# Kernel tuning notes

Measured on AMD Instinct MI355X. Metric: run time of the kernel, lower is better.

Reference implementation:

```python
import jax, jax.numpy as jnp
import numpy as np

B, N, A, T = 65536, 128, 32, 64


def setup_inputs() -> dict:
    key = jax.random.key(0)
    k1, k2, k3, k4 = jax.random.split(key, 4)
    traj = jax.random.normal(k1, (B, N, 3), dtype=jnp.float32)
    ref_x = jax.random.normal(k2, (A, 3), dtype=jnp.float32)
    ref_x = ref_x - jnp.mean(ref_x, axis=0, keepdims=True)  # centered ref, as in __init__
    align_idx = jnp.sort(jax.random.randint(k3, (A,), 0, N)).astype(jnp.int64)
    train_idx = jnp.sort(jax.random.randint(k4, (T,), 0, N)).astype(jnp.int64)
    return {"traj": traj, "ref_x": ref_x, "align_idx": align_idx, "train_idx": train_idx}


def reference(traj, ref_x, align_idx, train_idx):
    # --- Kabsch alignment ---
    sel = traj[:, align_idx, :]                      # [B, A, 3]
    x_c = jnp.mean(sel, axis=1, keepdims=True)       # [B, 1, 3]
    x0 = sel - x_c                                   # centered selection
    # prod = x0^T @ ref_x : [B, 3, 3]
    prod = jnp.einsum('bai,aj->bij', x0, ref_x)
    u, s, vh = jnp.linalg.svd(prod)                  # batched 3x3 SVD
    # proper-rotation sign fix (det of u @ vh), detached in the original
    sign = jax.lax.stop_gradient(jnp.sign(jnp.linalg.det(jnp.matmul(u, vh))))  # [B]
    d = jnp.stack([jnp.ones_like(sign), jnp.ones_like(sign), sign], axis=-1)   # [B, 3]
    rotate = jnp.matmul(u * d[:, None, :], vh)       # u @ diag(1,1,sign) @ vh, [B,3,3]
    aligned = jnp.matmul(traj - x_c, rotate)         # [B, N, 3]
    # --- select train atoms and flatten ---
    out = aligned[:, train_idx, :].reshape(traj.shape[0], -1)  # [B, T*3]
    return out
```

## Files before the change

kernel.cpp:

```cpp
#include <hip/hip_runtime.h>
#include <math.h>

#define N_ATOMS  128
#define A_ALIGN  32
#define T_TRAIN  64
#define ROWF     (N_ATOMS*3)
#define R4       (ROWF/4)
#define BPBLK    64
#define PPW      8

template<int p, int q, int r>
__device__ __forceinline__ void jrot(float Am[3][3], float Vm[3][3])
{
    float apq = Am[p][q];
    float app = Am[p][p];
    float aqq = Am[q][q];
    float tau = (aqq - app) / (2.0f * apq);
    float tt  = 1.0f / (fabsf(tau) + sqrtf(1.0f + tau * tau));
    float t   = copysignf(tt, tau);
    t = (fabsf(apq) > 1e-20f) ? t : 0.0f;
    float c = 1.0f / sqrtf(1.0f + t * t);
    float s = t * c;
    float arp = Am[r][p], arq = Am[r][q];
    float nrp = c * arp - s * arq;
    float nrq = s * arp + c * arq;
    Am[r][p] = nrp; Am[p][r] = nrp;
    Am[r][q] = nrq; Am[q][r] = nrq;
    Am[p][p] = app - t * apq;
    Am[q][q] = aqq + t * apq;
    Am[p][q] = 0.0f; Am[q][p] = 0.0f;
#pragma unroll
    for (int k = 0; k < 3; ++k) {
        float vp = Vm[k][p], vq = Vm[k][q];
        Vm[k][p] = c * vp - s * vq;
        Vm[k][q] = s * vp + c * vq;
    }
}

__device__ __forceinline__ float redu32(float v)
{
#pragma unroll
    for (int m = 16; m >= 1; m >>= 1)
        v += __shfl_xor(v, m, 32);
    return v;
}

__global__ __launch_bounds__(256)
void kabsch_onepass_kernel(const float* __restrict__ traj,
                           const float* __restrict__ ref_x,
                           const int*   __restrict__ align_idx,
                           const int*   __restrict__ train_idx,
                           float*       __restrict__ out,
                           int B)
{
    __shared__ float slice[4][2 * ROWF];
    __shared__ float Pbuf[BPBLK][12];

    const int tid = threadIdx.x;
    const int w  = tid >> 6;
    const int l  = tid & 63;
    const int h  = l >> 5;
    const int tp = l & 31;

    const long long bbase = (long long)blockIdx.x * BPBLK;

    const int   ia = align_idx[tp];
    const float rx = ref_x[tp*3+0], ry = ref_x[tp*3+1], rz = ref_x[tp*3+2];
    const int   ti0 = train_idx[tp];
    const int   ti1 = train_idx[tp + 32];

    const float4* __restrict__ g4 = (const float4*)traj;
    const long long maxf4 = (long long)B * R4;
    float4* s4 = (float4*)slice[w];
    const float* __restrict__ rb = &slice[w][h * ROWF];

#pragma unroll 1
    for (int it = 0; it < PPW; ++it) {
        int pl = w * PPW + it;
        long long b = bbase + (long long)pl * 2;
        if (b >= B) break;
        long long fb = b * R4;
        long long i0 = fb + l;        if (i0 >= maxf4) i0 = maxf4 - 1;
        long long i1 = fb + 64 + l;   if (i1 >= maxf4) i1 = maxf4 - 1;
        long long i2 = fb + 128 + l;  if (i2 >= maxf4) i2 = maxf4 - 1;
        float4 v0 = g4[i0];
        float4 v1 = g4[i1];
        float4 v2 = g4[i2];
        s4[l]       = v0;
        s4[64 + l]  = v1;
        s4[128 + l] = v2;

        float px = rb[ia*3+0], py = rb[ia*3+1], pz = rb[ia*3+2];

        float S00 = redu32(px*rx), S01 = redu32(px*ry), S02 = redu32(px*rz);
        float S10 = redu32(py*rx), S11 = redu32(py*ry), S12 = redu32(py*rz);
        float S20 = redu32(pz*rx), S21 = redu32(pz*ry), S22 = redu32(pz*rz);
        float xs0 = redu32(px), xs1 = redu32(py), xs2 = redu32(pz);
        float rs0 = redu32(rx), rs1 = redu32(ry), rs2 = redu32(rz);

        if (tp == 0 && (b + h) < B) {
            const float inv_a = 1.0f / (float)A_ALIGN;
            float c0 = xs0*inv_a, c1 = xs1*inv_a, c2 = xs2*inv_a;
            float4* o4 = (float4*)Pbuf[pl*2 + h];
            o4[0] = make_float4(S00 - c0*rs0, S01 - c0*rs1, S02 - c0*rs2,
                                S10 - c1*rs0);
            o4[1] = make_float4(S11 - c1*rs1, S12 - c1*rs2, S20 - c2*rs0,
                                S21 - c2*rs1);
            o4[2] = make_float4(S22 - c2*rs2, c0, c1, c2);
        }
    }
    __syncthreads();

    const int cw = blockIdx.x & 3;
    if ((tid >> 6) == cw && (bbase + (tid & 63)) < B) {
        const int r = tid & 63;
        float4* w4 = (float4*)Pbuf[r];
        float4 q0 = w4[0], q1 = w4[1], q2 = w4[2];
        float P00=q0.x, P01=q0.y, P02=q0.z, P10=q0.w;
        float P11=q1.x, P12=q1.y, P20=q1.z, P21=q1.w;
        float P22=q2.x, c0=q2.y, c1=q2.z, c2=q2.w;

        float Am[3][3], Vm[3][3];
        Am[0][0] = P00*P00 + P10*P10 + P20*P20;
        Am[0][1] = P00*P01 + P10*P11 + P20*P21;
        Am[0][2] = P00*P02 + P10*P12 + P20*P22;
        Am[1][1] = P01*P01 + P11*P11 + P21*P21;
        Am[1][2] = P01*P02 + P11*P12 + P21*P22;
        Am[2][2] = P02*P02 + P12*P12 + P22*P22;
        Am[1][0]=Am[0][1]; Am[2][0]=Am[0][2]; Am[2][1]=Am[1][2];
        Vm[0][0]=1.f; Vm[0][1]=0.f; Vm[0][2]=0.f;
        Vm[1][0]=0.f; Vm[1][1]=1.f; Vm[1][2]=0.f;
        Vm[2][0]=0.f; Vm[2][1]=0.f; Vm[2][2]=1.f;
#pragma unroll
        for (int sw = 0; sw < 6; ++sw) {
            jrot<0,1,2>(Am, Vm);
            jrot<0,2,1>(Am, Vm);
            jrot<1,2,0>(Am, Vm);
        }

        float l0 = Am[0][0], l1 = Am[1][1], l2 = Am[2][2];
        float v0x=Vm[0][0], v0y=Vm[1][0], v0z=Vm[2][0];
        float v1x=Vm[0][1], v1y=Vm[1][1], v1z=Vm[2][1];
        if (l0 < l1) { float t; t=l0;l0=l1;l1=t;
                       t=v0x;v0x=v1x;v1x=t; t=v0y;v0y=v1y;v1y=t; t=v0z;v0z=v1z;v1z=t; }
        { float v2x=Vm[0][2], v2y=Vm[1][2], v2z=Vm[2][2];
          if (l0 < l2) { float t; t=l0;l0=l2;l2=t;
                         t=v0x;v0x=v2x;v2x=t; t=v0y;v0y=v2y;v2y=t; t=v0z;v0z=v2z;v2z=t; }
          if (l1 < l2) { float t; t=l1;l1=l2;l2=t;
                         t=v1x;v1x=v2x;v2x=t; t=v1y;v1y=v2y;v2y=t; t=v1z;v1z=v2z;v2z=t; }
        }
        float v2x = v0y*v1z - v0z*v1y;
        float v2y = v0z*v1x - v0x*v1z;
        float v2z = v0x*v1y - v0y*v1x;
        float w0x = P00*v0x + P01*v0y + P02*v0z;
        float w0y = P10*v0x + P11*v0y + P12*v0z;
        float w0z = P20*v0x + P21*v0y + P22*v0z;
        float i0 = 1.0f / sqrtf(fmaxf(w0x*w0x+w0y*w0y+w0z*w0z, 1e-30f));
        float u0x=w0x*i0, u0y=w0y*i0, u0z=w0z*i0;
        float w1x = P00*v1x + P01*v1y + P02*v1z;
        float w1y = P10*v1x + P11*v1y + P12*v1z;
        float w1z = P20*v1x + P21*v1y + P22*v1z;
        float d01 = u0x*w1x + u0y*w1y + u0z*w1z;
        w1x -= d01*u0x; w1y -= d01*u0y; w1z -= d01*u0z;
        float i1 = 1.0f / sqrtf(fmaxf(w1x*w1x+w1y*w1y+w1z*w1z, 1e-30f));
        float u1x=w1x*i1, u1y=w1y*i1, u1z=w1z*i1;
        float u2x = u0y*u1z - u0z*u1y;
        float u2y = u0z*u1x - u0x*u1z;
        float u2z = u0x*u1y - u0y*u1x;

        w4[0] = make_float4(u0x*v0x + u1x*v1x + u2x*v2x,
                            u0x*v0y + u1x*v1y + u2x*v2y,
                            u0x*v0z + u1x*v1z + u2x*v2z,
                            u0y*v0x + u1y*v1x + u2y*v2x);
        w4[1] = make_float4(u0y*v0y + u1y*v1y + u2y*v2y,
                            u0y*v0z + u1y*v1z + u2y*v2z,
                            u0z*v0x + u1z*v1x + u2z*v2x,
                            u0z*v0y + u1z*v1y + u2z*v2y);
        w4[2] = make_float4(u0z*v0z + u1z*v1z + u2z*v2z, c0, c1, c2);
    }
    __syncthreads();

#pragma unroll 1
    for (int it = 0; it < PPW; ++it) {
        int pl = w * PPW + it;
        long long b = bbase + (long long)pl * 2;
        if (b >= B) break;
        long long fb = b * R4;
        long long i0 = fb + l;        if (i0 >= maxf4) i0 = maxf4 - 1;
        long long i1 = fb + 64 + l;   if (i1 >= maxf4) i1 = maxf4 - 1;
        long long i2 = fb + 128 + l;  if (i2 >= maxf4) i2 = maxf4 - 1;
        float4 v0 = g4[i0];
        float4 v1 = g4[i1];
        float4 v2 = g4[i2];
        s4[l]       = v0;
        s4[64 + l]  = v1;
        s4[128 + l] = v2;

        const long long brow = b + h;
        if (brow < B) {
            const float4* r4 = (const float4*)Pbuf[pl*2 + h];
            float4 q0 = r4[0], q1 = r4[1], q2 = r4[2];
            float R00=q0.x, R01=q0.y, R02=q0.z, R10=q0.w;
            float R11=q1.x, R12=q1.y, R20=q1.z, R21=q1.w;
            float R22=q2.x, c0=q2.y, c1=q2.z, c2=q2.w;
            {
                float x0 = rb[ti0*3+0]-c0, x1 = rb[ti0*3+1]-c1, x2 = rb[ti0*3+2]-c2;
                float3 y;
                y.x = x0*R00 + x1*R10 + x2*R20;
                y.y = x0*R01 + x1*R11 + x2*R21;
                y.z = x0*R02 + x1*R12 + x2*R22;
                *(float3*)(out + (brow * T_TRAIN + ti0*0 + tp) * 3) = y;
            }
            {
                float x0 = rb[ti1*3+0]-c0, x1 = rb[ti1*3+1]-c1, x2 = rb[ti1*3+2]-c2;
                float3 y;
                y.x = x0*R00 + x1*R10 + x2*R20;
                y.y = x0*R01 + x1*R11 + x2*R21;
                y.z = x0*R02 + x1*R12 + x2*R22;
                *(float3*)(out + (brow * T_TRAIN + tp + 32) * 3) = y;
            }
        }
    }
}

extern "C" void kernel_launch(void* const* d_in, const int* in_sizes, int n_in,
                              void* d_out, int out_size, void* d_ws, size_t ws_size,
                              hipStream_t stream)
{
    const float* traj      = (const float*)d_in[0];
    const float* ref_x     = (const float*)d_in[1];
    const int*   align_idx = (const int*)d_in[2];
    const int*   train_idx = (const int*)d_in[3];
    float* out = (float*)d_out;
    int B = in_sizes[0] / (N_ATOMS * 3);

    int nblk = (B + BPBLK - 1) / BPBLK;
    kabsch_onepass_kernel<<<dim3(nblk), dim3(256), 0, stream>>>(
        traj, ref_x, align_idx, train_idx, out, B);
}
```

Before: 52.05 us.

## Cache train-atom coordinates in registers to skip second trajectory read

The first pass now also copies each pair's train-atom coordinates from shared memory into per-iteration register arrays. The second pass uses these instead of re-reading the trajectory rows from global memory, which removes the second full read of traj. Rows per block drop from 64 to 32 (PPW 8 to 4) so the register arrays stay small, both loops are fully unrolled, and the reference-sum reduction is hoisted out of the loop. The cost is higher register use and twice as many blocks, each doing its own per-block setup and barrier work.

```diff
diff --git a/kernel.cpp b/kernel.cpp
--- a/kernel.cpp
+++ b/kernel.cpp
@@ -6,8 +6,8 @@
 #define T_TRAIN  64
 #define ROWF     (N_ATOMS*3)
 #define R4       (ROWF/4)
-#define BPBLK    64
-#define PPW      8
+#define BPBLK    32
+#define PPW      4
 
 template<int p, int q, int r>
 __device__ __forceinline__ void jrot(float Am[3][3], float Vm[3][3])
@@ -64,8 +64,8 @@
 
     const long long bbase = (long long)blockIdx.x * BPBLK;
 
-    const int   ia = align_idx[tp];
-    const float rx = ref_x[tp*3+0], ry = ref_x[tp*3+1], rz = ref_x[tp*3+2];
+    const int   ia  = align_idx[tp];
+    const float rx  = ref_x[tp*3+0], ry = ref_x[tp*3+1], rz = ref_x[tp*3+2];
     const int   ti0 = train_idx[tp];
     const int   ti1 = train_idx[tp + 32];
 
@@ -74,45 +74,52 @@
     float4* s4 = (float4*)slice[w];
     const float* __restrict__ rb = &slice[w][h * ROWF];
 
-#pragma unroll 1
+    const float rs0 = redu32(rx), rs1 = redu32(ry), rs2 = redu32(rz);
+
+    float t0x[PPW], t0y[PPW], t0z[PPW];
+    float t1x[PPW], t1y[PPW], t1z[PPW];
+
+#pragma unroll
     for (int it = 0; it < PPW; ++it) {
-        int pl = w * PPW + it;
-        long long b = bbase + (long long)pl * 2;
-        if (b >= B) break;
-        long long fb = b * R4;
-        long long i0 = fb + l;        if (i0 >= maxf4) i0 = maxf4 - 1;
-        long long i1 = fb + 64 + l;   if (i1 >= maxf4) i1 = maxf4 - 1;
-        long long i2 = fb + 128 + l;  if (i2 >= maxf4) i2 = maxf4 - 1;
-        float4 v0 = g4[i0];
-        float4 v1 = g4[i1];
-        float4 v2 = g4[i2];
-        s4[l]       = v0;
-        s4[64 + l]  = v1;
-        s4[128 + l] = v2;
-
-        float px = rb[ia*3+0], py = rb[ia*3+1], pz = rb[ia*3+2];
-
-        float S00 = redu32(px*rx), S01 = redu32(px*ry), S02 = redu32(px*rz);
-        float S10 = redu32(py*rx), S11 = redu32(py*ry), S12 = redu32(py*rz);
-        float S20 = redu32(pz*rx), S21 = redu32(pz*ry), S22 = redu32(pz*rz);
-        float xs0 = redu32(px), xs1 = redu32(py), xs2 = redu32(pz);
-        float rs0 = redu32(rx), rs1 = redu32(ry), rs2 = redu32(rz);
-
-        if (tp == 0 && (b + h) < B) {
-            const float inv_a = 1.0f / (float)A_ALIGN;
-            float c0 = xs0*inv_a, c1 = xs1*inv_a, c2 = xs2*inv_a;
-            float4* o4 = (float4*)Pbuf[pl*2 + h];
-            o4[0] = make_float4(S00 - c0*rs0, S01 - c0*rs1, S02 - c0*rs2,
-                                S10 - c1*rs0);
-            o4[1] = make_float4(S11 - c1*rs1, S12 - c1*rs2, S20 - c2*rs0,
-                                S21 - c2*rs1);
-            o4[2] = make_float4(S22 - c2*rs2, c0, c1, c2);
+        const int pl = w * PPW + it;
+        const long long b = bbase + (long long)pl * 2;
+        if (b < B) {
+            long long fb = b * R4;
+            long long i0 = fb + l;        if (i0 >= maxf4) i0 = maxf4 - 1;
+            long long i1 = fb + 64 + l;   if (i1 >= maxf4) i1 = maxf4 - 1;
+            long long i2 = fb + 128 + l;  if (i2 >= maxf4) i2 = maxf4 - 1;
+            float4 v0 = g4[i0];
+            float4 v1 = g4[i1];
+            float4 v2 = g4[i2];
+            s4[l]       = v0;
+            s4[64 + l]  = v1;
+            s4[128 + l] = v2;
+
+            float px = rb[ia*3+0], py = rb[ia*3+1], pz = rb[ia*3+2];
+            t0x[it] = rb[ti0*3+0]; t0y[it] = rb[ti0*3+1]; t0z[it] = rb[ti0*3+2];
+            t1x[it] = rb[ti1*3+0]; t1y[it] = rb[ti1*3+1]; t1z[it] = rb[ti1*3+2];
+
+            float S00 = redu32(px*rx), S01 = redu32(px*ry), S02 = redu32(px*rz);
+            float S10 = redu32(py*rx), S11 = redu32(py*ry), S12 = redu32(py*rz);
+            float S20 = redu32(pz*rx), S21 = redu32(pz*ry), S22 = redu32(pz*rz);
+            float xs0 = redu32(px), xs1 = redu32(py), xs2 = redu32(pz);
+
+            if (tp == 0 && (b + h) < B) {
+                const float inv_a = 1.0f / (float)A_ALIGN;
+                float c0 = xs0*inv_a, c1 = xs1*inv_a, c2 = xs2*inv_a;
+                float4* o4 = (float4*)Pbuf[pl*2 + h];
+                o4[0] = make_float4(S00 - c0*rs0, S01 - c0*rs1, S02 - c0*rs2,
+                                    S10 - c1*rs0);
+                o4[1] = make_float4(S11 - c1*rs1, S12 - c1*rs2, S20 - c2*rs0,
+                                    S21 - c2*rs1);
+                o4[2] = make_float4(S22 - c2*rs2, c0, c1, c2);
+            }
         }
     }
     __syncthreads();
 
     const int cw = blockIdx.x & 3;
-    if ((tid >> 6) == cw && (bbase + (tid & 63)) < B) {
+    if ((tid >> 6) == cw && (tid & 63) < BPBLK && (bbase + (tid & 63)) < B) {
         const int r = tid & 63;
         float4* w4 = (float4*)Pbuf[r];
         float4 q0 = w4[0], q1 = w4[1], q2 = w4[2];
@@ -180,39 +187,27 @@
     }
     __syncthreads();
 
-#pragma unroll 1
+#pragma unroll
     for (int it = 0; it < PPW; ++it) {
-        int pl = w * PPW + it;
-        long long b = bbase + (long long)pl * 2;
-        if (b >= B) break;
-        long long fb = b * R4;
-        long long i0 = fb + l;        if (i0 >= maxf4) i0 = maxf4 - 1;
-        long long i1 = fb + 64 + l;   if (i1 >= maxf4) i1 = maxf4 - 1;
-        long long i2 = fb + 128 + l;  if (i2 >= maxf4) i2 = maxf4 - 1;
-        float4 v0 = g4[i0];
-        float4 v1 = g4[i1];
-        float4 v2 = g4[i2];
-        s4[l]       = v0;
-        s4[64 + l]  = v1;
-        s4[128 + l] = v2;
-
+        const int pl = w * PPW + it;
+        const long long b = bbase + (long long)pl * 2;
         const long long brow = b + h;
         if (brow < B) {
-            const float4* r4 = (const float4*)Pbuf[pl*2 + h];
-            float4 q0 = r4[0], q1 = r4[1], q2 = r4[2];
+            const float4* r4p = (const float4*)Pbuf[pl*2 + h];
+            float4 q0 = r4p[0], q1 = r4p[1], q2 = r4p[2];
             float R00=q0.x, R01=q0.y, R02=q0.z, R10=q0.w;
             float R11=q1.x, R12=q1.y, R20=q1.z, R21=q1.w;
             float R22=q2.x, c0=q2.y, c1=q2.z, c2=q2.w;
             {
-                float x0 = rb[ti0*3+0]-c0, x1 = rb[ti0*3+1]-c1, x2 = rb[ti0*3+2]-c2;
+                float x0 = t0x[it]-c0, x1 = t0y[it]-c1, x2 = t0z[it]-c2;
                 float3 y;
                 y.x = x0*R00 + x1*R10 + x2*R20;
                 y.y = x0*R01 + x1*R11 + x2*R21;
                 y.z = x0*R02 + x1*R12 + x2*R22;
-                *(float3*)(out + (brow * T_TRAIN + ti0*0 + tp) * 3) = y;
+                *(float3*)(out + (brow * T_TRAIN + tp) * 3) = y;
             }
             {
-                float x0 = rb[ti1*3+0]-c0, x1 = rb[ti1*3+1]-c1, x2 = rb[ti1*3+2]-c2;
+                float x0 = t1x[it]-c0, x1 = t1y[it]-c1, x2 = t1z[it]-c2;
                 float3 y;
                 y.x = x0*R00 + x1*R10 + x2*R20;
                 y.y = x0*R01 + x1*R11 + x2*R21;
```

After: 47.96 us. 1.09x faster.
